# Kernel optimization log

Measured on AMD Instinct MI355X. Metric: run time of the kernel, lower is better.

## Reference

```python
import jax, jax.numpy as jnp
import numpy as np

B, S, IN_DIM, HID = 8, 2048, 1024, 1024


def setup_inputs() -> dict:
    key = jax.random.key(0)
    k1, k2, k3, k4, k5 = jax.random.split(key, 5)
    vec = jax.random.normal(k1, (B, S, IN_DIM), dtype=jnp.float32)
    # nn.Linear-style init scale
    wq_w = jax.random.normal(k2, (HID, IN_DIM), dtype=jnp.float32) / np.sqrt(IN_DIM)
    wq_b = jax.random.normal(k3, (HID,), dtype=jnp.float32) * 0.02
    lin_w = jax.random.normal(k4, (1, HID), dtype=jnp.float32) / np.sqrt(HID)
    lin_b = jax.random.normal(k5, (1,), dtype=jnp.float32) * 0.02
    return {"vec": vec, "wq_w": wq_w, "wq_b": wq_b, "lin_w": lin_w, "lin_b": lin_b}


def reference(vec, wq_w, wq_b, lin_w, lin_b):
    # NOTE: the original forward applies self.wq to BOTH q and k (wk/nq/nk unused).
    q = jnp.einsum('bsi,hi->bsh', vec, wq_w) + wq_b          # [B,S,H]
    ret = jnp.einsum('bsx,bsy->bxy', q, q)                    # [B,H,H] bilinear
    ret = jax.nn.relu(ret)
    out = jnp.einsum('bxy,y->bx', ret, lin_w[0]) + lin_b[0]   # Linear(H,1) -> [B,H]
    return out
```

## Files before the change

kernel.cpp:

```cpp
#include <hip/hip_runtime.h>


typedef short     bf16x8 __attribute__((ext_vector_type(8)));
typedef unsigned short u16x8 __attribute__((ext_vector_type(8)));
typedef float     f32x4 __attribute__((ext_vector_type(4)));
typedef long long i64;

__device__ inline unsigned short f2bf(float f) {
  unsigned int u = __float_as_uint(f);
  u += 0x7fffu + ((u >> 16) & 1u);
  return (unsigned short)(u >> 16);
}

__device__ inline u16x8 pack8(float4 a, float4 b) {
  u16x8 r;
  r[0] = f2bf(a.x); r[1] = f2bf(a.y); r[2] = f2bf(a.z); r[3] = f2bf(a.w);
  r[4] = f2bf(b.x); r[5] = f2bf(b.y); r[6] = f2bf(b.z); r[7] = f2bf(b.w);
  return r;
}

__device__ inline unsigned char f2fp8(float v) {
  int pk = __builtin_amdgcn_cvt_pk_fp8_f32(v, v, 0, false);
  return (unsigned char)(pk & 0xff);
}

__device__ inline void async16(void* lds, const void* g) {
  __builtin_amdgcn_global_load_lds(
      (const __attribute__((address_space(1))) void*)g,
      (__attribute__((address_space(3))) void*)lds,
      16, 0, 0);
}

__global__ __launch_bounds__(256) void prep(
    const float* __restrict__ vec, unsigned short* __restrict__ vecbf,
    const float* __restrict__ wq,  unsigned short* __restrict__ wqbf,
    const float* __restrict__ lin_b, float* __restrict__ out)
{
  const int gid = blockIdx.x * 256 + threadIdx.x;
  if (blockIdx.x < 8192) {
    const float4* s = (const float4*)(vec + (size_t)gid * 8);
    float4 a = s[0], b = s[1];
    *(u16x8*)(vecbf + (size_t)gid * 8) = pack8(a, b);
    if (gid < 8192) out[gid] = lin_b[0];
  } else {
    const int i = gid - 8192 * 256;
    const float4* s = (const float4*)(wq + (size_t)i * 8);
    float4 a = s[0], b = s[1];
    *(u16x8*)(wqbf + (size_t)i * 8) = pack8(a, b);
  }
}

__global__ void init_out(float* __restrict__ out, const float* __restrict__ lin_b) {
  int i = blockIdx.x * 256 + threadIdx.x;
  if (i < 8192) out[i] = lin_b[0];
}

__global__ __launch_bounds__(512, 2) void gemm_q8p(
    const unsigned short* __restrict__ A, const unsigned short* __restrict__ Bm,
    const float* __restrict__ bias, unsigned char* __restrict__ qT8)
{
  __shared__ unsigned short As[2][256 * 64];
  __shared__ unsigned short Bs[2][256 * 64];

  const int m0 = blockIdx.y * 256;
  const int n0 = blockIdx.x * 256;
  const int t    = threadIdx.x;
  const int lane = t & 63;
  const int wave = t >> 6;
  const int wm2  = (wave >> 2) * 64;
  const int wn2  = (wave & 3) * 32;
  const int quad = lane >> 4;
  const int lrow = lane & 15;

  const int srow = t >> 3;
  const int gch  = (t & 7) ^ (srow & 7);
  const unsigned short* gA = A  + (size_t)(m0 + srow) * 1024 + gch * 8;
  const unsigned short* gB = Bm + (size_t)(n0 + srow) * 1024 + gch * 8;

#define VMCNT(N) asm volatile("s_waitcnt vmcnt(" #N ")" ::: "memory")
#define BARR __builtin_amdgcn_s_barrier()

#define STAGE_A(SLOT, H, KT) do { \
  _Pragma("unroll") for (int p = 0; p < 2; ++p) \
    async16(&As[SLOT][((H)*128 + p*64)*64 + t*8], \
            gA + (size_t)((H)*128 + p*64)*1024 + (KT)*64); \
} while (0)

#define STAGE_B(SLOT, H, KT) do { \
  _Pragma("unroll") for (int p = 0; p < 2; ++p) \
    async16(&Bs[SLOT][((H)*128 + p*64)*64 + t*8], \
            gB + (size_t)((H)*128 + p*64)*1024 + (KT)*64); \
} while (0)

#define LDA_HALF(S, MH) do { \
  _Pragma("unroll") for (int f = 0; f < 4; ++f) \
  _Pragma("unroll") for (int kk = 0; kk < 2; ++kk) \
    a_[f][kk] = *(const bf16x8*)&As[S][((MH)*128 + wm2 + f*16 + lrow)*64 + \
                                       (((kk*4 + quad) ^ (lrow & 7)) * 8)]; \
} while (0)

#define LDB_HALF(S, NH, BREG) do { \
  _Pragma("unroll") for (int g = 0; g < 2; ++g) \
  _Pragma("unroll") for (int kk = 0; kk < 2; ++kk) \
    BREG[g][kk] = *(const bf16x8*)&Bs[S][((NH)*128 + wn2 + g*16 + lrow)*64 + \
                                         (((kk*4 + quad) ^ (lrow & 7)) * 8)]; \
} while (0)

#define MFMAQ(MH, NH, BREG) do { \
  __builtin_amdgcn_s_setprio(1); \
  _Pragma("unroll") for (int kk = 0; kk < 2; ++kk) \
  _Pragma("unroll") for (int f = 0; f < 4; ++f) \
  _Pragma("unroll") for (int g = 0; g < 2; ++g) \
    acc[MH][f][NH][g] = __builtin_amdgcn_mfma_f32_16x16x32_bf16( \
        a_[f][kk], BREG[g][kk], acc[MH][f][NH][g], 0, 0, 0); \
  __builtin_amdgcn_s_setprio(0); \
} while (0)

  f32x4 acc[2][4][2][2];
#pragma unroll
  for (int i = 0; i < 2; ++i)
#pragma unroll
    for (int f = 0; f < 4; ++f)
#pragma unroll
      for (int j = 0; j < 2; ++j)
#pragma unroll
        for (int g = 0; g < 2; ++g) acc[i][f][j][g] = (f32x4){0.f, 0.f, 0.f, 0.f};

  bf16x8 a_[4][2], b0_[2][2], b1_[2][2];

  STAGE_A(0, 0, 0);
  STAGE_B(0, 0, 0);
  STAGE_B(0, 1, 0);
  STAGE_A(0, 1, 0);
  VMCNT(4);
  BARR;

#pragma unroll 1
  for (int kt = 0; kt < 15; ++kt) {
    const int s  = kt & 1;
    const int so = s ^ 1;

    LDA_HALF(s, 0);
    LDB_HALF(s, 0, b0_);
    STAGE_A(so, 0, kt + 1);
    VMCNT(4);
    BARR;
    MFMAQ(0, 0, b0_);
    BARR;

    LDB_HALF(s, 1, b1_);
    STAGE_B(so, 0, kt + 1);
    VMCNT(4);
    BARR;
    MFMAQ(0, 1, b1_);
    BARR;

    LDA_HALF(s, 1);
    STAGE_B(so, 1, kt + 1);
    VMCNT(4);
    BARR;
    MFMAQ(1, 0, b0_);
    BARR;

    STAGE_A(so, 1, kt + 1);
    VMCNT(4);
    BARR;
    MFMAQ(1, 1, b1_);
    BARR;
  }

  LDA_HALF(1, 0);
  LDB_HALF(1, 0, b0_);
  VMCNT(2);
  BARR;
  MFMAQ(0, 0, b0_);
  BARR;

  LDB_HALF(1, 1, b1_);
  VMCNT(0);
  BARR;
  MFMAQ(0, 1, b1_);
  BARR;

  LDA_HALF(1, 1);
  MFMAQ(1, 0, b0_);
  MFMAQ(1, 1, b1_);

#pragma unroll
  for (int mh = 0; mh < 2; ++mh)
#pragma unroll
    for (int f = 0; f < 4; ++f)
#pragma unroll
      for (int r = 0; r < 4; ++r) {
        const int m = m0 + mh * 128 + wm2 + f * 16 + quad * 4 + r;
        const float bv = bias[m];
        unsigned char* row = qT8 + (size_t)m * 16384 + n0;
#pragma unroll
        for (int nh = 0; nh < 2; ++nh)
#pragma unroll
          for (int g = 0; g < 2; ++g)
            row[nh * 128 + wn2 + g * 16 + lrow] = f2fp8(acc[mh][f][nh][g][r] + bv);
      }

#undef VMCNT
#undef BARR
#undef STAGE_A
#undef STAGE_B
#undef LDA_HALF
#undef LDB_HALF
#undef MFMAQ
}

__global__ __launch_bounds__(256) void gemm_q_fused(
    const float* __restrict__ Wq, const float* __restrict__ V,
    const float* __restrict__ bias, unsigned char* __restrict__ qT8)
{
  __shared__ unsigned short As[128 * 32];
  __shared__ unsigned short Bs[128 * 32];

  const int m0 = blockIdx.y * 128;
  const int n0 = blockIdx.x * 128;
  const int t    = threadIdx.x;
  const int lane = t & 63;
  const int wave = t >> 6;
  const int wm = (wave >> 1) * 64;
  const int wn = (wave & 1) * 64;
  const int quad = lane >> 4;
  const int lrow = lane & 15;

  const int sr = t >> 1;
  const int sc = (t & 1) << 4;
  const float* gA = Wq + (size_t)(m0 + sr) * 1024 + sc;
  const float* gB = V  + (size_t)(n0 + sr) * 1024 + sc;

  f32x4 acc[4][4];
#pragma unroll
  for (int i = 0; i < 4; ++i)
#pragma unroll
    for (int j = 0; j < 4; ++j) acc[i][j] = (f32x4){0.f, 0.f, 0.f, 0.f};

  for (int k0 = 0; k0 < 1024; k0 += 32) {
    const float4* a4 = (const float4*)(gA + k0);
    const float4* b4 = (const float4*)(gB + k0);
    float4 av0 = a4[0], av1 = a4[1], av2 = a4[2], av3 = a4[3];
    float4 bv0 = b4[0], bv1 = b4[1], bv2 = b4[2], bv3 = b4[3];
    *(u16x8*)&As[sr * 32 + sc]     = pack8(av0, av1);
    *(u16x8*)&As[sr * 32 + sc + 8] = pack8(av2, av3);
    *(u16x8*)&Bs[sr * 32 + sc]     = pack8(bv0, bv1);
    *(u16x8*)&Bs[sr * 32 + sc + 8] = pack8(bv2, bv3);
    __syncthreads();

    bf16x8 af[4], bfr[4];
#pragma unroll
    for (int i = 0; i < 4; ++i)
      af[i] = *(const bf16x8*)&As[(wm + i * 16 + lrow) * 32 + quad * 8];
#pragma unroll
    for (int j = 0; j < 4; ++j)
      bfr[j] = *(const bf16x8*)&Bs[(wn + j * 16 + lrow) * 32 + quad * 8];
#pragma unroll
    for (int i = 0; i < 4; ++i)
#pragma unroll
      for (int j = 0; j < 4; ++j)
        acc[i][j] = __builtin_amdgcn_mfma_f32_16x16x32_bf16(af[i], bfr[j], acc[i][j], 0, 0, 0);
    __syncthreads();
  }

#pragma unroll
  for (int i = 0; i < 4; ++i) {
    const int mb = m0 + wm + i * 16 + quad * 4;
#pragma unroll
    for (int r = 0; r < 4; ++r) {
      const float bv = bias[mb + r];
#pragma unroll
      for (int j = 0; j < 4; ++j) {
        const int n = n0 + wn + j * 16 + lrow;
        qT8[(size_t)(mb + r) * 16384 + n] = f2fp8(acc[i][j][r] + bv);
      }
    }
  }
}

__global__ __launch_bounds__(256) void syrk_half8(
    const unsigned char* __restrict__ qT8, const float* __restrict__ W,
    float* __restrict__ out)
{
  __shared__ unsigned char As[128 * 128];
  __shared__ unsigned char Bs[64 * 128];

  const int bb   = blockIdx.z;
  const int pair = blockIdx.x >> 1;
  const int yh   = blockIdx.x & 1;
  int tx = 0;
  while ((tx + 1) * (tx + 2) / 2 <= pair) ++tx;
  const int ty = pair - tx * (tx + 1) / 2;
  const int x0 = tx * 128;
  const int y0 = ty * 128 + yh * 64;
  const bool diag = (tx == ty);

  const int t    = threadIdx.x;
  const int lane = t & 63;
  const int wave = t >> 6;
  const int wm = (wave >> 1) * 64;
  const int wn = (wave & 1) * 32;
  const int quad = lane >> 4;
  const int lrow = lane & 15;

  const int srow = t >> 3;
  const int g16  = (t & 7) ^ (srow & 7);
  const size_t cb = (size_t)bb * 2048 + g16 * 16;
  const unsigned char* gA = qT8 + (size_t)(x0 + srow) * 16384 + cb;
  const unsigned char* gB = qT8 + (size_t)(y0 + srow) * 16384 + cb;

  f32x4 acc[4][2];
#pragma unroll
  for (int i = 0; i < 4; ++i)
#pragma unroll
    for (int j = 0; j < 2; ++j) acc[i][j] = (f32x4){0.f, 0.f, 0.f, 0.f};

  for (int k0 = 0; k0 < 2048; k0 += 128) {
#pragma unroll
    for (int p = 0; p < 4; ++p)
      async16(&As[p * 4096 + t * 16], gA + (size_t)p * 32 * 16384 + k0);
#pragma unroll
    for (int p = 0; p < 2; ++p)
      async16(&Bs[p * 4096 + t * 16], gB + (size_t)p * 32 * 16384 + k0);
    __syncthreads();

#pragma unroll
    for (int kk = 0; kk < 4; ++kk) {
      const int c = kk * 4 + quad;
      const int off = (((c >> 1) ^ (lrow & 7)) << 4) + (c & 1) * 8;
      i64 af[4], bfr[2];
#pragma unroll
      for (int i = 0; i < 4; ++i)
        af[i] = *(const i64*)&As[(wm + i * 16 + lrow) * 128 + off];
#pragma unroll
      for (int j = 0; j < 2; ++j)
        bfr[j] = *(const i64*)&Bs[(wn + j * 16 + lrow) * 128 + off];
#pragma unroll
      for (int i = 0; i < 4; ++i)
#pragma unroll
        for (int j = 0; j < 2; ++j)
          acc[i][j] = __builtin_amdgcn_mfma_f32_16x16x32_fp8_fp8(af[i], bfr[j], acc[i][j], 0, 0, 0);
    }
    __syncthreads();
  }

  float* ob = out + bb * 1024;

  float wv[2];
#pragma unroll
  for (int j = 0; j < 2; ++j) wv[j] = W[y0 + wn + j * 16 + lrow];

#pragma unroll
  for (int i = 0; i < 4; ++i) {
#pragma unroll
    for (int r = 0; r < 4; ++r) {
      float p = 0.f;
#pragma unroll
      for (int j = 0; j < 2; ++j) {
        float v = acc[i][j][r];
        v = v > 0.f ? v : 0.f;
        p += v * wv[j];
      }
#pragma unroll
      for (int off = 1; off < 16; off <<= 1) p += __shfl_xor(p, off, 64);
      if (lrow == 0)
        atomicAdd(&ob[x0 + wm + i * 16 + quad * 4 + r], p);
    }
  }

  if (!diag) {
    float wx[4][4];
#pragma unroll
    for (int i = 0; i < 4; ++i)
#pragma unroll
      for (int r = 0; r < 4; ++r)
        wx[i][r] = W[x0 + wm + i * 16 + quad * 4 + r];

#pragma unroll
    for (int j = 0; j < 2; ++j) {
      float pc = 0.f;
#pragma unroll
      for (int i = 0; i < 4; ++i)
#pragma unroll
        for (int r = 0; r < 4; ++r) {
          float v = acc[i][j][r];
          v = v > 0.f ? v : 0.f;
          pc += v * wx[i][r];
        }
      pc += __shfl_xor(pc, 16, 64);
      pc += __shfl_xor(pc, 32, 64);
      if (quad == 0)
        atomicAdd(&ob[y0 + wn + j * 16 + lrow], pc);
    }
  }
}

extern "C" void kernel_launch(void* const* d_in, const int* in_sizes, int n_in,
                              void* d_out, int out_size, void* d_ws, size_t ws_size,
                              hipStream_t stream) {
  const float* vec   = (const float*)d_in[0];
  const float* wq_w  = (const float*)d_in[1];
  const float* wq_b  = (const float*)d_in[2];
  const float* lin_w = (const float*)d_in[3];
  const float* lin_b = (const float*)d_in[4];
  float* out = (float*)d_out;

  unsigned char* qT8 = (unsigned char*)d_ws;
  const size_t need = (size_t)(16 + 32 + 2) * 1024 * 1024;

  if (ws_size >= need) {
    unsigned short* vecbf = (unsigned short*)((char*)d_ws + (size_t)16 * 1024 * 1024);
    unsigned short* wqbf  = vecbf + (size_t)16 * 1024 * 1024;
    prep<<<dim3(8192 + 512), dim3(256), 0, stream>>>(vec, vecbf, wq_w, wqbf, lin_b, out);
    gemm_q8p<<<dim3(64, 4), dim3(512), 0, stream>>>(wqbf, vecbf, wq_b, qT8);
  } else {
    init_out<<<dim3(32), dim3(256), 0, stream>>>(out, lin_b);
    gemm_q_fused<<<dim3(128, 8), dim3(256), 0, stream>>>(wq_w, vec, wq_b, qT8);
  }
  syrk_half8<<<dim3(72, 1, 8), dim3(256), 0, stream>>>(qT8, lin_w, out);
}
```

Baseline: 168.6 us.

## Double-buffer SYRK LDS tiles and reschedule GEMM prefetch stages

The SYRK kernel gets double-buffered LDS tiles, so the next K-tile's async global-to-LDS copies are issued before computing the current one, overlapping load latency with fp8 MFMA work. The bf16 GEMM main loop is reordered to issue prefetch stages ahead of the LDS reads, with looser vmcnt waits and fewer barriers per iteration. BARR now carries compiler memory fences. This doubles SYRK LDS use, which may reduce occupancy, and relies on the vmcnt counts matching the number of outstanding async copies.

```diff
diff --git a/kernel.cpp b/kernel.cpp
--- a/kernel.cpp
+++ b/kernel.cpp
@@ -5,6 +5,10 @@
 typedef unsigned short u16x8 __attribute__((ext_vector_type(8)));
 typedef float     f32x4 __attribute__((ext_vector_type(4)));
 typedef long long i64;
+
+#define FENCE asm volatile("" ::: "memory")
+#define BARR  do { FENCE; __builtin_amdgcn_s_barrier(); FENCE; } while (0)
+#define VMCNT(N) asm volatile("s_waitcnt vmcnt(" #N ")" ::: "memory")
 
 __device__ inline unsigned short f2bf(float f) {
   unsigned int u = __float_as_uint(f);
@@ -77,9 +81,6 @@
   const unsigned short* gA = A  + (size_t)(m0 + srow) * 1024 + gch * 8;
   const unsigned short* gB = Bm + (size_t)(n0 + srow) * 1024 + gch * 8;
 
-#define VMCNT(N) asm volatile("s_waitcnt vmcnt(" #N ")" ::: "memory")
-#define BARR __builtin_amdgcn_s_barrier()
-
 #define STAGE_A(SLOT, H, KT) do { \
   _Pragma("unroll") for (int p = 0; p < 2; ++p) \
     async16(&As[SLOT][((H)*128 + p*64)*64 + t*8], \
@@ -132,56 +133,50 @@
   STAGE_B(0, 0, 0);
   STAGE_B(0, 1, 0);
   STAGE_A(0, 1, 0);
-  VMCNT(4);
-  BARR;
 
 #pragma unroll 1
   for (int kt = 0; kt < 15; ++kt) {
     const int s  = kt & 1;
     const int so = s ^ 1;
 
+    STAGE_A(so, 0, kt + 1);
+    STAGE_B(so, 0, kt + 1);
+    VMCNT(8);
+    BARR;
     LDA_HALF(s, 0);
     LDB_HALF(s, 0, b0_);
-    STAGE_A(so, 0, kt + 1);
-    VMCNT(4);
-    BARR;
     MFMAQ(0, 0, b0_);
     BARR;
 
+    STAGE_B(so, 1, kt + 1);
+    VMCNT(8);
+    BARR;
     LDB_HALF(s, 1, b1_);
-    STAGE_B(so, 0, kt + 1);
-    VMCNT(4);
-    BARR;
     MFMAQ(0, 1, b1_);
     BARR;
 
+    STAGE_A(so, 1, kt + 1);
+    VMCNT(8);
+    BARR;
     LDA_HALF(s, 1);
-    STAGE_B(so, 1, kt + 1);
-    VMCNT(4);
-    BARR;
     MFMAQ(1, 0, b0_);
-    BARR;
-
-    STAGE_A(so, 1, kt + 1);
-    VMCNT(4);
-    BARR;
     MFMAQ(1, 1, b1_);
     BARR;
   }
 
+  VMCNT(4);
+  BARR;
   LDA_HALF(1, 0);
   LDB_HALF(1, 0, b0_);
+  MFMAQ(0, 0, b0_);
+
   VMCNT(2);
   BARR;
-  MFMAQ(0, 0, b0_);
-  BARR;
-
   LDB_HALF(1, 1, b1_);
+  MFMAQ(0, 1, b1_);
+
   VMCNT(0);
   BARR;
-  MFMAQ(0, 1, b1_);
-  BARR;
-
   LDA_HALF(1, 1);
   MFMAQ(1, 0, b0_);
   MFMAQ(1, 1, b1_);
@@ -202,8 +197,6 @@
             row[nh * 128 + wn2 + g * 16 + lrow] = f2fp8(acc[mh][f][nh][g][r] + bv);
       }
 
-#undef VMCNT
-#undef BARR
 #undef STAGE_A
 #undef STAGE_B
 #undef LDA_HALF
@@ -284,8 +277,8 @@
     const unsigned char* __restrict__ qT8, const float* __restrict__ W,
     float* __restrict__ out)
 {
-  __shared__ unsigned char As[128 * 128];
-  __shared__ unsigned char Bs[64 * 128];
+  __shared__ unsigned char As[2][128 * 128];
+  __shared__ unsigned char Bs[2][64 * 128];
 
   const int bb   = blockIdx.z;
   const int pair = blockIdx.x >> 1;
@@ -311,40 +304,52 @@
   const unsigned char* gA = qT8 + (size_t)(x0 + srow) * 16384 + cb;
   const unsigned char* gB = qT8 + (size_t)(y0 + srow) * 16384 + cb;
 
+#define SSTAGE(SLOT, KT) do { \
+  _Pragma("unroll") for (int p = 0; p < 4; ++p) \
+    async16(&As[SLOT][p * 4096 + t * 16], gA + (size_t)p * 32 * 16384 + (KT) * 128); \
+  _Pragma("unroll") for (int p = 0; p < 2; ++p) \
+    async16(&Bs[SLOT][p * 4096 + t * 16], gB + (size_t)p * 32 * 16384 + (KT) * 128); \
+} while (0)
+
+#define SYRK_COMPUTE(S) do { \
+  _Pragma("unroll") for (int kk = 0; kk < 4; ++kk) { \
+    const int c = kk * 4 + quad; \
+    const int off = (((c >> 1) ^ (lrow & 7)) << 4) + (c & 1) * 8; \
+    i64 af[4], bfr[2]; \
+    _Pragma("unroll") for (int i = 0; i < 4; ++i) \
+      af[i] = *(const i64*)&As[S][(wm + i * 16 + lrow) * 128 + off]; \
+    _Pragma("unroll") for (int j = 0; j < 2; ++j) \
+      bfr[j] = *(const i64*)&Bs[S][(wn + j * 16 + lrow) * 128 + off]; \
+    _Pragma("unroll") for (int i = 0; i < 4; ++i) \
+      _Pragma("unroll") for (int j = 0; j < 2; ++j) \
+        acc[i][j] = __builtin_amdgcn_mfma_f32_16x16x32_fp8_fp8(af[i], bfr[j], acc[i][j], 0, 0, 0); \
+  } \
+} while (0)
+
   f32x4 acc[4][2];
 #pragma unroll
   for (int i = 0; i < 4; ++i)
 #pragma unroll
     for (int j = 0; j < 2; ++j) acc[i][j] = (f32x4){0.f, 0.f, 0.f, 0.f};
 
-  for (int k0 = 0; k0 < 2048; k0 += 128) {
-#pragma unroll
-    for (int p = 0; p < 4; ++p)
-      async16(&As[p * 4096 + t * 16], gA + (size_t)p * 32 * 16384 + k0);
-#pragma unroll
-    for (int p = 0; p < 2; ++p)
-      async16(&Bs[p * 4096 + t * 16], gB + (size_t)p * 32 * 16384 + k0);
-    __syncthreads();
-
-#pragma unroll
-    for (int kk = 0; kk < 4; ++kk) {
-      const int c = kk * 4 + quad;
-      const int off = (((c >> 1) ^ (lrow & 7)) << 4) + (c & 1) * 8;
-      i64 af[4], bfr[2];
-#pragma unroll
-      for (int i = 0; i < 4; ++i)
-        af[i] = *(const i64*)&As[(wm + i * 16 + lrow) * 128 + off];
-#pragma unroll
-      for (int j = 0; j < 2; ++j)
-        bfr[j] = *(const i64*)&Bs[(wn + j * 16 + lrow) * 128 + off];
-#pragma unroll
-      for (int i = 0; i < 4; ++i)
-#pragma unroll
-        for (int j = 0; j < 2; ++j)
-          acc[i][j] = __builtin_amdgcn_mfma_f32_16x16x32_fp8_fp8(af[i], bfr[j], acc[i][j], 0, 0, 0);
-    }
-    __syncthreads();
-  }
+  SSTAGE(0, 0);
+
+#pragma unroll 1
+  for (int kt = 0; kt < 15; ++kt) {
+    const int s = kt & 1;
+    SSTAGE(s ^ 1, kt + 1);
+    VMCNT(6);
+    BARR;
+    SYRK_COMPUTE(s);
+    BARR;
+  }
+
+  VMCNT(0);
+  BARR;
+  SYRK_COMPUTE(1);
+
+#undef SSTAGE
+#undef SYRK_COMPUTE
 
   float* ob = out + bb * 1024;
 
```

Measured after the change: 171.5 us. About the same (+1.7%).
